# Kernel tuning notes

Hardware: AMD Instinct MI355X
Metric: run time of the kernel (lower is better)

The kernel has to match this reference:

```python
import jax, jax.numpy as jnp
import numpy as np

HIDDEN = 1024
N_HEADS = 16
N_KV_HEADS = 4
HEAD_DIM = HIDDEN // N_HEADS  # 64
GROUPS = N_HEADS // N_KV_HEADS  # 4


def setup_inputs() -> dict:
    key = jax.random.key(0)
    k1, k2, k3, k4 = jax.random.split(key, 4)
    B, T = 2, 2048
    s = 0.02
    x = jax.random.normal(k1, (B, T, HIDDEN), dtype=jnp.float32)
    Wq = jax.random.normal(k2, (HIDDEN, N_HEADS * HEAD_DIM), dtype=jnp.float32) * s
    Wkv = jax.random.normal(k3, (HIDDEN, 2 * N_KV_HEADS * HEAD_DIM), dtype=jnp.float32) * s
    Wo = jax.random.normal(k4, (N_HEADS * HEAD_DIM, HIDDEN), dtype=jnp.float32) * s
    return {"x": x, "Wq": Wq, "Wkv": Wkv, "Wo": Wo}


def reference(x, Wq, Wkv, Wo):
    B, T, _ = x.shape
    scale = HEAD_DIM ** -0.5
    q = (x @ Wq).reshape(B, T, N_HEADS, HEAD_DIM).transpose(0, 2, 1, 3)  # [B,H,T,D]
    kv = x @ Wkv
    k, v = jnp.split(kv, 2, axis=-1)
    k = k.reshape(B, T, N_KV_HEADS, HEAD_DIM).transpose(0, 2, 1, 3)  # [B,Hkv,T,D]
    v = v.reshape(B, T, N_KV_HEADS, HEAD_DIM).transpose(0, 2, 1, 3)
    # repeat_interleave over head dim -> [B,H,T,D]
    k = jnp.repeat(k, GROUPS, axis=1)
    v = jnp.repeat(v, GROUPS, axis=1)
    scores = jnp.einsum("bhqd,bhkd->bhqk", q, k) * scale
    causal = jnp.triu(jnp.ones((T, T), dtype=bool), k=1)
    scores = jnp.where(causal[None, None], -jnp.inf, scores)
    w = jax.nn.softmax(scores, axis=-1)
    out = jnp.einsum("bhqk,bhkd->bhqd", w, v)
    out = out.transpose(0, 2, 1, 3).reshape(B, T, N_HEADS * HEAD_DIM)
    return out @ Wo
```

## Files before the change

### kernel.cpp

```cpp
#include <hip/hip_runtime.h>

using bf16x8 = __attribute__((ext_vector_type(8))) __bf16;
using f32x4  = __attribute__((ext_vector_type(4))) float;

__device__ __forceinline__ short f2bf(float f) {
  unsigned u = __builtin_bit_cast(unsigned, f);
  u += 0x7fffu + ((u >> 16) & 1u);
  return (short)(u >> 16);
}

__device__ __forceinline__ void gll16(const void* g, void* l) {
  __builtin_amdgcn_global_load_lds((const __attribute__((address_space(1))) unsigned*)g,
                                   (__attribute__((address_space(3))) unsigned*)l, 16, 0, 0);
}

__global__ __launch_bounds__(256) void fused_pre(const float* __restrict__ x,
                                                 const float* __restrict__ Wq,
                                                 const float* __restrict__ Wkv,
                                                 const float* __restrict__ Wo,
                                                 short* __restrict__ xb,
                                                 short* __restrict__ Wqkvt,
                                                 short* __restrict__ Wot) {
  const int bx = blockIdx.x, tid = threadIdx.x;
  if (bx < 4096) {
    int i = (bx * 256 + tid) * 4;
    float4 f = *(const float4*)(&x[i]);
    short4 o;
    o.x = f2bf(f.x); o.y = f2bf(f.y); o.z = f2bf(f.z); o.w = f2bf(f.w);
    *(short4*)(&xb[i]) = o;
    return;
  }
  __shared__ short tile[32][33];
  const float* src; short* dst; int C, ti;
  if (bx < 5120)      { src = Wq;  dst = Wqkvt;               C = 1024; ti = bx - 4096; }
  else if (bx < 5632) { src = Wkv; dst = Wqkvt + 1024 * 1024; C = 512;  ti = bx - 5120; }
  else                { src = Wo;  dst = Wot;                 C = 1024; ti = bx - 5632; }
  int ctiles = C >> 5;
  int c0 = (ti % ctiles) * 32, r0 = (ti / ctiles) * 32;
  int tx = tid & 31, ty = tid >> 5;
  for (int i = ty; i < 32; i += 8)
    tile[i][tx] = f2bf(src[(r0 + i) * C + c0 + tx]);
  __syncthreads();
  for (int i = ty; i < 32; i += 8)
    dst[(c0 + i) * 1024L + r0 + tx] = tile[tx][i];
}

template <int N, int K, int NT, bool OUT_BF16, bool WRITE_VT>
__global__ __launch_bounds__(256) void gemm_bt(const short* __restrict__ A,
                                               const short* __restrict__ Bt,
                                               void* __restrict__ Cout,
                                               short* __restrict__ Vt) {
  __shared__ __attribute__((aligned(16))) short sA[2][64 * 64];
  __shared__ __attribute__((aligned(16))) short sB[2][32 * NT * 64];
  const int tid  = threadIdx.x;
  const int bm   = blockIdx.y * 64, bn = blockIdx.x * (32 * NT);
  const int wave = tid >> 6, lane = tid & 63;
  const int wm = (wave >> 1) * 32, wn = (wave & 1) * (16 * NT);
  const int qd = lane >> 4, c16 = lane & 15;

  f32x4 acc[2][NT] = {};

  auto stage = [&](int it, int d) {
    int k0 = it * 64;
#pragma unroll
    for (int i = 0; i < 2; i++) {
      int c = i * 256 + tid;
      int r = c >> 3, cc = c & 7;
      gll16(&A[(bm + r) * (long)K + k0 + ((cc ^ (r & 7)) * 8)],
            &sA[d][(i * 256 + wave * 64) * 8]);
    }
#pragma unroll
    for (int i = 0; i < NT; i++) {
      int c = i * 256 + tid;
      int r = c >> 3, cc = c & 7;
      gll16(&Bt[(bn + r) * (long)K + k0 + ((cc ^ (r & 7)) * 8)],
            &sB[d][(i * 256 + wave * 64) * 8]);
    }
  };

  constexpr int niter = K >> 6;
  stage(0, 0);
#pragma unroll
  for (int it = 0; it < niter; it++) {
    const int cur = it & 1;
    asm volatile("" ::: "memory");
    __builtin_amdgcn_s_barrier();
    if (it + 1 < niter) {
      stage(it + 1, cur ^ 1);
      if constexpr (NT == 3) asm volatile("s_waitcnt vmcnt(5)" ::: "memory");
      else                   asm volatile("s_waitcnt vmcnt(4)" ::: "memory");
    } else {
      asm volatile("s_waitcnt vmcnt(0)" ::: "memory");
    }
    __builtin_amdgcn_s_barrier();
    asm volatile("" ::: "memory");

    bf16x8 af[2][2], bfr[NT][2];
#pragma unroll
    for (int mt = 0; mt < 2; mt++) {
      int rr = wm + mt * 16 + c16;
#pragma unroll
      for (int ks = 0; ks < 2; ks++)
        af[mt][ks] = *(const bf16x8*)(&sA[cur][rr * 64 + (((ks * 4 + qd) ^ (rr & 7)) * 8)]);
    }
#pragma unroll
    for (int nt = 0; nt < NT; nt++) {
      int rr = wn + nt * 16 + c16;
#pragma unroll
      for (int ks = 0; ks < 2; ks++)
        bfr[nt][ks] = *(const bf16x8*)(&sB[cur][rr * 64 + (((ks * 4 + qd) ^ (rr & 7)) * 8)]);
    }
#pragma unroll
    for (int ks = 0; ks < 2; ks++)
#pragma unroll
      for (int mt = 0; mt < 2; mt++)
#pragma unroll
        for (int nt = 0; nt < NT; nt++)
          acc[mt][nt] = __builtin_amdgcn_mfma_f32_16x16x32_bf16(af[mt][ks], bfr[nt][ks],
                                                                acc[mt][nt], 0, 0, 0);
  }

#pragma unroll
  for (int mt = 0; mt < 2; mt++)
#pragma unroll
    for (int nt = 0; nt < NT; nt++) {
      long row0 = bm + wm + mt * 16 + qd * 4;
      long col  = bn + wn + nt * 16 + c16;
      short4 p;
#pragma unroll
      for (int r = 0; r < 4; r++) {
        float v = acc[mt][nt][r];
        if constexpr (OUT_BF16) ((short*)Cout)[(row0 + r) * N + col] = f2bf(v);
        else                    ((float*)Cout)[(row0 + r) * N + col] = v;
        if constexpr (WRITE_VT)
          ((short*)&p)[r] = f2bf(v);
      }
      if constexpr (WRITE_VT) {
        if (col >= 1280) {
          int d = (int)col - 1280;
          int b = (int)(row0 >> 11), t = (int)(row0 & 2047);
          *(short4*)(&Vt[((long)(b * 256 + d)) * 2048 + t]) = p;
        }
      }
    }
}

#define CSOFT 0.18033688f
#define CMAX  (CSOFT * 12.0f)

__global__ __launch_bounds__(256, 4) void attn_kernel(const short* __restrict__ QKV,
                                                      const short* __restrict__ Vt,
                                                      short* __restrict__ Aout) {
  const int bx = blockIdx.x;
  const int qt = (bx < 512) ? (127 - (bx >> 3)) : ((bx >> 3) - 64);
  const int kvh = (bx >> 1) & 3, b = bx & 1;
  const int bkv = b * 4 + kvh;
  const int tid = threadIdx.x;
  const int w = tid >> 6, lane = tid & 63;
  const int qd = lane >> 4, c16 = lane & 15;
  const int h = kvh * 4 + w;
  const int q0 = qt * 16;

  __shared__ __attribute__((aligned(16))) short sK[2][64 * 64];
  __shared__ __attribute__((aligned(16))) short sVt[64 * 64];
  __shared__ __attribute__((aligned(16))) short sP[4][16 * 72];

  const int r0 = tid >> 3, cc = tid & 7;
  const int sw = (cc ^ (r0 & 7)) * 8;
  const short* pK0 = QKV + ((long)(b * 2048 + r0)) * 1536 + 1024 + kvh * 64 + sw;
  const short* pK1 = pK0 + 32 * 1536;
  const short* pV0 = Vt + ((long)(bkv * 64 + r0)) * 2048 + sw;
  const short* pV1 = pV0 + 32 * 2048;
  short* const dK0[2] = { (short*)&sK[0][(w * 64) * 8],       (short*)&sK[1][(w * 64) * 8] };
  short* const dK1[2] = { (short*)&sK[0][(256 + w * 64) * 8], (short*)&sK[1][(256 + w * 64) * 8] };
  short* const dV0 = (short*)&sVt[(w * 64) * 8];
  short* const dV1 = (short*)&sVt[(256 + w * 64) * 8];

  auto stageK = [&](int d) {
    gll16(pK0, dK0[d]); gll16(pK1, dK1[d]);
    pK0 += 64 * 1536;   pK1 += 64 * 1536;
  };
  auto stageV = [&]() {
    gll16(pV0, dV0); gll16(pV1, dV1);
    pV0 += 64;       pV1 += 64;
  };

  stageK(0);

  bf16x8 qf[2];
  {
    long tok = (long)b * 2048 + q0 + c16;
#pragma unroll
    for (int ks = 0; ks < 2; ks++)
      qf[ks] = *(const bf16x8*)(&QKV[tok * 1536 + h * 64 + ks * 32 + qd * 8]);
  }

  f32x4 Ot[4] = {};
  float l_i = 0.f;

  const int ntiles = (qt >> 2) + 1;
  for (int kt = 0; kt < ntiles; kt++) {
    const int cur = kt & 1;
    asm volatile("" ::: "memory");
    __builtin_amdgcn_s_barrier();
    stageV();
    if (kt + 1 < ntiles) {
      stageK(cur ^ 1);
      asm volatile("s_waitcnt vmcnt(4)" ::: "memory");
    } else {
      asm volatile("s_waitcnt vmcnt(2)" ::: "memory");
    }
    __builtin_amdgcn_s_barrier();
    asm volatile("" ::: "memory");

    f32x4 St[4];
#pragma unroll
    for (int jc = 0; jc < 4; jc++) {
      int rr = jc * 16 + c16;
      bf16x8 kf0 = *(const bf16x8*)(&sK[cur][rr * 64 + ((0 + qd) ^ (rr & 7)) * 8]);
      bf16x8 kf1 = *(const bf16x8*)(&sK[cur][rr * 64 + ((4 + qd) ^ (rr & 7)) * 8]);
      f32x4 z = {};
      z = __builtin_amdgcn_mfma_f32_16x16x32_bf16(kf0, qf[0], z, 0, 0, 0);
      z = __builtin_amdgcn_mfma_f32_16x16x32_bf16(kf1, qf[1], z, 0, 0, 0);
      St[jc] = z;
    }

    if (kt == ntiles - 1) {
      int qg = q0 + c16 - kt * 64;
#pragma unroll
      for (int jc = 0; jc < 4; jc++)
#pragma unroll
        for (int r = 0; r < 4; r++)
          if (jc * 16 + qd * 4 + r > qg) St[jc][r] = -3e38f;
    }

    {
      float rs = 0.f;
#pragma unroll
      for (int jc = 0; jc < 4; jc++) {
        unsigned u4[4];
#pragma unroll
        for (int r = 0; r < 4; r++) {
          float p = exp2f(fmaf(CSOFT, St[jc][r], -CMAX));
          u4[r] = __builtin_bit_cast(unsigned, p) & 0xffff0000u;
          rs += __builtin_bit_cast(float, u4[r]);
        }
        int2 pk;
        pk.x = (int)((u4[0] >> 16) | u4[1]);
        pk.y = (int)((u4[2] >> 16) | u4[3]);
        *(int2*)(&sP[w][c16 * 72 + jc * 16 + qd * 4]) = pk;
      }
      l_i += rs;
    }
    asm volatile("s_waitcnt lgkmcnt(0)" ::: "memory");

    if (kt + 1 < ntiles) asm volatile("s_waitcnt vmcnt(2)" ::: "memory");
    else                 asm volatile("s_waitcnt vmcnt(0)" ::: "memory");
    __builtin_amdgcn_s_barrier();
    asm volatile("" ::: "memory");

#pragma unroll
    for (int ks2 = 0; ks2 < 2; ks2++) {
      bf16x8 pf = *(const bf16x8*)(&sP[w][c16 * 72 + ks2 * 32 + qd * 8]);
#pragma unroll
      for (int dt = 0; dt < 4; dt++) {
        int rr = dt * 16 + c16;
        bf16x8 vf = *(const bf16x8*)(&sVt[rr * 64 + (((ks2 * 4 + qd) ^ (rr & 7)) * 8)]);
        Ot[dt] = __builtin_amdgcn_mfma_f32_16x16x32_bf16(vf, pf, Ot[dt], 0, 0, 0);
      }
    }
  }

  {
    float l = l_i;
    l += __shfl_xor(l, 16, 64);
    l += __shfl_xor(l, 32, 64);
    float inv = 1.f / l;
    long tok = (long)b * 2048 + q0 + c16;
#pragma unroll
    for (int dt = 0; dt < 4; dt++) {
      short4 o;
      o.x = f2bf(Ot[dt][0] * inv);
      o.y = f2bf(Ot[dt][1] * inv);
      o.z = f2bf(Ot[dt][2] * inv);
      o.w = f2bf(Ot[dt][3] * inv);
      *(short4*)(&Aout[tok * 1024 + h * 64 + dt * 16 + qd * 4]) = o;
    }
  }
}

extern "C" void kernel_launch(void* const* d_in, const int* in_sizes, int n_in,
                              void* d_out, int out_size, void* d_ws, size_t ws_size,
                              hipStream_t stream) {
  const float* x   = (const float*)d_in[0];
  const float* Wq  = (const float*)d_in[1];
  const float* Wkv = (const float*)d_in[2];
  const float* Wo  = (const float*)d_in[3];

  char* ws = (char*)d_ws;
  short* xb    = (short*)(ws);
  short* Wqkvt = (short*)(ws + 8388608);
  short* Wot   = (short*)(ws + 11534336);
  short* QKV   = (short*)(ws + 13631488);
  short* attn  = (short*)(ws + 26214400);
  short* Vtb   = (short*)d_out;

  fused_pre<<<dim3(6656), 256, 0, stream>>>(x, Wq, Wkv, Wo, xb, Wqkvt, Wot);

  gemm_bt<1536, 1024, 3, true, true><<<dim3(16, 64), 256, 0, stream>>>(xb, Wqkvt, QKV, Vtb);

  attn_kernel<<<dim3(1024), 256, 0, stream>>>(QKV, Vtb, attn);

  gemm_bt<1024, 1024, 2, false, false><<<dim3(16, 64), 256, 0, stream>>>(attn, Wot, d_out, nullptr);
}
```

Before: 150.4 us.

## Load K and V fragments directly from global memory instead of LDS staging

Removes the double-buffered LDS staging of K and V tiles (global_load_lds plus block barriers) from the attention kernel. Each wave now loads its MFMA K and V fragments straight from global memory into registers. The second V half is issued after the softmax so its latency overlaps with that work. This drops the per-tile barriers and LDS traffic, but each of the four waves in a block now reads the same K/V data redundantly from cache, and there is no longer any prefetch of the next tile. The launch-bounds occupancy hint is also relaxed.

```diff
diff --git a/kernel.cpp b/kernel.cpp
--- a/kernel.cpp
+++ b/kernel.cpp
@@ -148,9 +148,9 @@
 #define CSOFT 0.18033688f
 #define CMAX  (CSOFT * 12.0f)
 
-__global__ __launch_bounds__(256, 4) void attn_kernel(const short* __restrict__ QKV,
-                                                      const short* __restrict__ Vt,
-                                                      short* __restrict__ Aout) {
+__global__ __launch_bounds__(256) void attn_kernel(const short* __restrict__ QKV,
+                                                   const short* __restrict__ Vt,
+                                                   short* __restrict__ Aout) {
   const int bx = blockIdx.x;
   const int qt = (bx < 512) ? (127 - (bx >> 3)) : ((bx >> 3) - 64);
   const int kvh = (bx >> 1) & 3, b = bx & 1;
@@ -161,31 +161,10 @@
   const int h = kvh * 4 + w;
   const int q0 = qt * 16;
 
-  __shared__ __attribute__((aligned(16))) short sK[2][64 * 64];
-  __shared__ __attribute__((aligned(16))) short sVt[64 * 64];
   __shared__ __attribute__((aligned(16))) short sP[4][16 * 72];
 
-  const int r0 = tid >> 3, cc = tid & 7;
-  const int sw = (cc ^ (r0 & 7)) * 8;
-  const short* pK0 = QKV + ((long)(b * 2048 + r0)) * 1536 + 1024 + kvh * 64 + sw;
-  const short* pK1 = pK0 + 32 * 1536;
-  const short* pV0 = Vt + ((long)(bkv * 64 + r0)) * 2048 + sw;
-  const short* pV1 = pV0 + 32 * 2048;
-  short* const dK0[2] = { (short*)&sK[0][(w * 64) * 8],       (short*)&sK[1][(w * 64) * 8] };
-  short* const dK1[2] = { (short*)&sK[0][(256 + w * 64) * 8], (short*)&sK[1][(256 + w * 64) * 8] };
-  short* const dV0 = (short*)&sVt[(w * 64) * 8];
-  short* const dV1 = (short*)&sVt[(256 + w * 64) * 8];
-
-  auto stageK = [&](int d) {
-    gll16(pK0, dK0[d]); gll16(pK1, dK1[d]);
-    pK0 += 64 * 1536;   pK1 += 64 * 1536;
-  };
-  auto stageV = [&]() {
-    gll16(pV0, dV0); gll16(pV1, dV1);
-    pV0 += 64;       pV1 += 64;
-  };
-
-  stageK(0);
+  const short* pK = QKV + ((long)(b * 2048 + c16)) * 1536 + 1024 + kvh * 64 + qd * 8;
+  const short* pV = Vt + ((long)(bkv * 64 + c16)) * 2048 + qd * 8;
 
   bf16x8 qf[2];
   {
@@ -200,28 +179,24 @@
 
   const int ntiles = (qt >> 2) + 1;
   for (int kt = 0; kt < ntiles; kt++) {
-    const int cur = kt & 1;
-    asm volatile("" ::: "memory");
-    __builtin_amdgcn_s_barrier();
-    stageV();
-    if (kt + 1 < ntiles) {
-      stageK(cur ^ 1);
-      asm volatile("s_waitcnt vmcnt(4)" ::: "memory");
-    } else {
-      asm volatile("s_waitcnt vmcnt(2)" ::: "memory");
-    }
-    __builtin_amdgcn_s_barrier();
-    asm volatile("" ::: "memory");
+    bf16x8 kf[4][2];
+#pragma unroll
+    for (int jc = 0; jc < 4; jc++) {
+      const short* p = pK + jc * (16 * 1536);
+      kf[jc][0] = *(const bf16x8*)(p);
+      kf[jc][1] = *(const bf16x8*)(p + 32);
+    }
+    bf16x8 vf0[4];
+#pragma unroll
+    for (int dt = 0; dt < 4; dt++)
+      vf0[dt] = *(const bf16x8*)(pV + dt * (16 * 2048));
 
     f32x4 St[4];
 #pragma unroll
     for (int jc = 0; jc < 4; jc++) {
-      int rr = jc * 16 + c16;
-      bf16x8 kf0 = *(const bf16x8*)(&sK[cur][rr * 64 + ((0 + qd) ^ (rr & 7)) * 8]);
-      bf16x8 kf1 = *(const bf16x8*)(&sK[cur][rr * 64 + ((4 + qd) ^ (rr & 7)) * 8]);
       f32x4 z = {};
-      z = __builtin_amdgcn_mfma_f32_16x16x32_bf16(kf0, qf[0], z, 0, 0, 0);
-      z = __builtin_amdgcn_mfma_f32_16x16x32_bf16(kf1, qf[1], z, 0, 0, 0);
+      z = __builtin_amdgcn_mfma_f32_16x16x32_bf16(kf[jc][0], qf[0], z, 0, 0, 0);
+      z = __builtin_amdgcn_mfma_f32_16x16x32_bf16(kf[jc][1], qf[1], z, 0, 0, 0);
       St[jc] = z;
     }
 
@@ -252,23 +227,24 @@
       }
       l_i += rs;
     }
+
+    bf16x8 vf1[4];
+#pragma unroll
+    for (int dt = 0; dt < 4; dt++)
+      vf1[dt] = *(const bf16x8*)(pV + dt * (16 * 2048) + 32);
+
     asm volatile("s_waitcnt lgkmcnt(0)" ::: "memory");
-
-    if (kt + 1 < ntiles) asm volatile("s_waitcnt vmcnt(2)" ::: "memory");
-    else                 asm volatile("s_waitcnt vmcnt(0)" ::: "memory");
-    __builtin_amdgcn_s_barrier();
-    asm volatile("" ::: "memory");
-
-#pragma unroll
-    for (int ks2 = 0; ks2 < 2; ks2++) {
-      bf16x8 pf = *(const bf16x8*)(&sP[w][c16 * 72 + ks2 * 32 + qd * 8]);
-#pragma unroll
-      for (int dt = 0; dt < 4; dt++) {
-        int rr = dt * 16 + c16;
-        bf16x8 vf = *(const bf16x8*)(&sVt[rr * 64 + (((ks2 * 4 + qd) ^ (rr & 7)) * 8)]);
-        Ot[dt] = __builtin_amdgcn_mfma_f32_16x16x32_bf16(vf, pf, Ot[dt], 0, 0, 0);
-      }
-    }
+    bf16x8 pf0 = *(const bf16x8*)(&sP[w][c16 * 72 + 0 * 32 + qd * 8]);
+    bf16x8 pf1 = *(const bf16x8*)(&sP[w][c16 * 72 + 1 * 32 + qd * 8]);
+#pragma unroll
+    for (int dt = 0; dt < 4; dt++)
+      Ot[dt] = __builtin_amdgcn_mfma_f32_16x16x32_bf16(vf0[dt], pf0, Ot[dt], 0, 0, 0);
+#pragma unroll
+    for (int dt = 0; dt < 4; dt++)
+      Ot[dt] = __builtin_amdgcn_mfma_f32_16x16x32_bf16(vf1[dt], pf1, Ot[dt], 0, 0, 0);
+
+    pK += 64 * 1536;
+    pV += 64;
   }
 
   {
```

New measurement: 233.1 us. 55.0% more time.

## Replace LDS-staged GEMM with single-wave register-only GEMM tiles

Applied to the files above, without the earlier changes.

Replaces the 256-thread shared-memory double-buffered GEMM with a one-wave-per-block kernel that loads A and B fragments straight from global memory into registers and computes a 64x64 tile with 16 MFMA accumulators. This removes LDS staging, barriers and async copy waits, but gives up data sharing between waves. Global loads become strided 16-byte per-lane accesses with no software pipelining, so latency hiding depends on occupancy and the cache.

```diff
diff --git a/kernel.cpp b/kernel.cpp
--- a/kernel.cpp
+++ b/kernel.cpp
@@ -45,87 +45,46 @@
     dst[(c0 + i) * 1024L + r0 + tx] = tile[tx][i];
 }
 
-template <int N, int K, int NT, bool OUT_BF16, bool WRITE_VT>
-__global__ __launch_bounds__(256) void gemm_bt(const short* __restrict__ A,
-                                               const short* __restrict__ Bt,
-                                               void* __restrict__ Cout,
-                                               short* __restrict__ Vt) {
-  __shared__ __attribute__((aligned(16))) short sA[2][64 * 64];
-  __shared__ __attribute__((aligned(16))) short sB[2][32 * NT * 64];
-  const int tid  = threadIdx.x;
-  const int bm   = blockIdx.y * 64, bn = blockIdx.x * (32 * NT);
-  const int wave = tid >> 6, lane = tid & 63;
-  const int wm = (wave >> 1) * 32, wn = (wave & 1) * (16 * NT);
+template <int N, int K, bool OUT_BF16, bool WRITE_VT>
+__global__ __launch_bounds__(64, 2) void flat_gemm(const short* __restrict__ A,
+                                                   const short* __restrict__ Bt,
+                                                   void* __restrict__ Cout,
+                                                   short* __restrict__ Vt) {
+  const int lane = threadIdx.x;
+  const int bm = blockIdx.y * 64, bn = blockIdx.x * 64;
   const int qd = lane >> 4, c16 = lane & 15;
 
-  f32x4 acc[2][NT] = {};
-
-  auto stage = [&](int it, int d) {
-    int k0 = it * 64;
-#pragma unroll
-    for (int i = 0; i < 2; i++) {
-      int c = i * 256 + tid;
-      int r = c >> 3, cc = c & 7;
-      gll16(&A[(bm + r) * (long)K + k0 + ((cc ^ (r & 7)) * 8)],
-            &sA[d][(i * 256 + wave * 64) * 8]);
-    }
-#pragma unroll
-    for (int i = 0; i < NT; i++) {
-      int c = i * 256 + tid;
-      int r = c >> 3, cc = c & 7;
-      gll16(&Bt[(bn + r) * (long)K + k0 + ((cc ^ (r & 7)) * 8)],
-            &sB[d][(i * 256 + wave * 64) * 8]);
-    }
-  };
-
-  constexpr int niter = K >> 6;
-  stage(0, 0);
-#pragma unroll
-  for (int it = 0; it < niter; it++) {
-    const int cur = it & 1;
-    asm volatile("" ::: "memory");
-    __builtin_amdgcn_s_barrier();
-    if (it + 1 < niter) {
-      stage(it + 1, cur ^ 1);
-      if constexpr (NT == 3) asm volatile("s_waitcnt vmcnt(5)" ::: "memory");
-      else                   asm volatile("s_waitcnt vmcnt(4)" ::: "memory");
-    } else {
-      asm volatile("s_waitcnt vmcnt(0)" ::: "memory");
-    }
-    __builtin_amdgcn_s_barrier();
-    asm volatile("" ::: "memory");
-
-    bf16x8 af[2][2], bfr[NT][2];
-#pragma unroll
-    for (int mt = 0; mt < 2; mt++) {
-      int rr = wm + mt * 16 + c16;
-#pragma unroll
-      for (int ks = 0; ks < 2; ks++)
-        af[mt][ks] = *(const bf16x8*)(&sA[cur][rr * 64 + (((ks * 4 + qd) ^ (rr & 7)) * 8)]);
-    }
-#pragma unroll
-    for (int nt = 0; nt < NT; nt++) {
-      int rr = wn + nt * 16 + c16;
-#pragma unroll
-      for (int ks = 0; ks < 2; ks++)
-        bfr[nt][ks] = *(const bf16x8*)(&sB[cur][rr * 64 + (((ks * 4 + qd) ^ (rr & 7)) * 8)]);
-    }
+  f32x4 acc[4][4] = {};
+
+  const short* pA = A  + (long)(bm + c16) * K + qd * 8;
+  const short* pB = Bt + (long)(bn + c16) * K + qd * 8;
+
+#pragma unroll
+  for (int it = 0; it < (K >> 6); it++) {
+    bf16x8 af[4][2], bfr[4][2];
+#pragma unroll
+    for (int t = 0; t < 4; t++)
+#pragma unroll
+      for (int ks = 0; ks < 2; ks++) {
+        af[t][ks]  = *(const bf16x8*)(pA + (long)t * 16 * K + it * 64 + ks * 32);
+        bfr[t][ks] = *(const bf16x8*)(pB + (long)t * 16 * K + it * 64 + ks * 32);
+      }
 #pragma unroll
     for (int ks = 0; ks < 2; ks++)
 #pragma unroll
-      for (int mt = 0; mt < 2; mt++)
-#pragma unroll
-        for (int nt = 0; nt < NT; nt++)
+      for (int mt = 0; mt < 4; mt++)
+#pragma unroll
+        for (int nt = 0; nt < 4; nt++)
           acc[mt][nt] = __builtin_amdgcn_mfma_f32_16x16x32_bf16(af[mt][ks], bfr[nt][ks],
                                                                 acc[mt][nt], 0, 0, 0);
   }
 
 #pragma unroll
-  for (int mt = 0; mt < 2; mt++)
-#pragma unroll
-    for (int nt = 0; nt < NT; nt++) {
-      long row0 = bm + wm + mt * 16 + qd * 4;
-      long col  = bn + wn + nt * 16 + c16;
+  for (int mt = 0; mt < 4; mt++)
+#pragma unroll
+    for (int nt = 0; nt < 4; nt++) {
+      long row0 = bm + mt * 16 + qd * 4;
+      long col  = bn + nt * 16 + c16;
       short4 p;
 #pragma unroll
       for (int r = 0; r < 4; r++) {
@@ -307,9 +266,9 @@
 
   fused_pre<<<dim3(6656), 256, 0, stream>>>(x, Wq, Wkv, Wo, xb, Wqkvt, Wot);
 
-  gemm_bt<1536, 1024, 3, true, true><<<dim3(16, 64), 256, 0, stream>>>(xb, Wqkvt, QKV, Vtb);
+  flat_gemm<1536, 1024, true, true><<<dim3(24, 64), 64, 0, stream>>>(xb, Wqkvt, QKV, Vtb);
 
   attn_kernel<<<dim3(1024), 256, 0, stream>>>(QKV, Vtb, attn);
 
-  gemm_bt<1024, 1024, 2, false, false><<<dim3(16, 64), 256, 0, stream>>>(attn, Wot, d_out, nullptr);
-}
+  flat_gemm<1024, 1024, false, false><<<dim3(16, 64), 64, 0, stream>>>(attn, Wot, d_out, nullptr);
+}
```

New measurement: 204.8 us. 36.2% more time.
